# Kernel tuning notes

Measured on AMD Instinct MI355X. Metric: run time of the kernel, lower is better.

Reference implementation:

```python
import jax, jax.numpy as jnp
import numpy as np

# Image grid matching params nImgX/nImgY; nImgZ == nDctY (slice-wise 2D parallel-beam BP)
NIMG_X = 512
NIMG_Y = 512


def _backproject(proj):
    """Pixel-driven 2D parallel-beam backprojection applied per slice.

    proj: (nView, Z, nDct) sinogram (views over [0, pi), unit detector/pixel spacing,
    detector and image both centered). Returns vol: (Z, NIMG_Y, NIMG_X),
    scaled by pi/nView (the weighting the original module applies, cf. its backward).
    """
    nView, Z, nDct = proj.shape
    thetas = jnp.arange(nView, dtype=jnp.float32) * (np.pi / nView)
    xs = jnp.arange(NIMG_X, dtype=jnp.float32) - (NIMG_X - 1) / 2.0
    ys = jnp.arange(NIMG_Y, dtype=jnp.float32) - (NIMG_Y - 1) / 2.0
    ctr = (nDct - 1) / 2.0

    def step(vol, inp):
        p, c, s = inp                      # p: (Z, nDct)
        t = xs[None, :] * c + ys[:, None] * s + ctr   # (Y, X) detector coordinate
        i0 = jnp.floor(t).astype(jnp.int32)
        w = t - i0.astype(jnp.float32)
        v0 = (i0 >= 0) & (i0 < nDct)
        v1 = ((i0 + 1) >= 0) & ((i0 + 1) < nDct)
        i0c = jnp.clip(i0, 0, nDct - 1)
        i1c = jnp.clip(i0 + 1, 0, nDct - 1)
        g0 = p[:, i0c]                      # (Z, Y, X) gather
        g1 = p[:, i1c]
        contrib = g0 * jnp.where(v0, 1.0 - w, 0.0)[None] + g1 * jnp.where(v1, w, 0.0)[None]
        return vol + contrib, None

    vol0 = jnp.zeros((Z, NIMG_Y, NIMG_X), dtype=proj.dtype)
    vol, _ = jax.lax.scan(step, vol0, (proj, jnp.cos(thetas), jnp.sin(thetas)))
    return vol * jnp.float32(np.pi / nView)


def setup_inputs() -> dict:
    key = jax.random.key(0)
    # sinogram: (nDctY=32 slices, 1, nView=720, nDctX=1024)
    x = jax.random.normal(key, (32, 1, 720, 1024), dtype=jnp.float32)
    return {"x": x}


def reference(x):
    # original: squeeze -> (Z, nView, nDct) -> transpose(1,0,2) -> (nView, Z, nDct)
    proj = jnp.transpose(x[:, 0], (1, 0, 2))
    vol = _backproject(proj)               # (Z, NIMG_Y, NIMG_X)
    return vol[:, None, :, :]              # (nImgZ, 1, nImgY, nImgX)
```

## Files before the change

### kernel.cpp

```cpp
#include <hip/hip_runtime.h>
#include <math.h>

#define NVIEW 720
#define NDCT  1024
#define NZ    32
#define NX    512
#define NY    512

#define NR 24
#define RSTRIDE 20

typedef unsigned int uint;

#if __has_builtin(__builtin_amdgcn_fdot2)
#define USE_FDOT2 1
typedef _Float16 half2v __attribute__((ext_vector_type(2)));
#else
#define USE_FDOT2 0
#endif

__device__ __forceinline__ uint f2bf_rne(float f) {
    uint u = __float_as_uint(f);
    return (u + 0x7fffu + ((u >> 16) & 1u)) >> 16;
}

__device__ __forceinline__ uint pack_word(float a, float b) {
#if USE_FDOT2
    union { _Float16 h[2]; uint u; } r;
    r.h[0] = (_Float16)a;
    r.h[1] = (_Float16)(b - a);
    return r.u;
#else
    uint lo = f2bf_rne(b - a);
    uint u  = (f2bf_rne(a) << 16) | lo;
    uint up = u + 0x10000u, um = u - 0x10000u;
    float e0 = fabsf(__uint_as_float(u)  - a);
    float e1 = fabsf(__uint_as_float(up) - a);
    float e2 = fabsf(__uint_as_float(um) - a);
    if (e1 < e0) { u = up; e0 = e1; }
    if (e2 < e0) { u = um; }
    return u;
#endif
}

__global__ __launch_bounds__(64) void pack_kernel(const float* __restrict__ x,
                                                  uint* __restrict__ packed) {
    __shared__ uint tr[64 * 33];
    const int l  = threadIdx.x;
    const int v  = blockIdx.x;
    const int ib = blockIdx.y * 64;
    const bool last = (ib + 64 >= NDCT);
    const float* rowbase = x + (size_t)v * NDCT + ib;

    float pre = 0.0f;
    if (l < NZ && !last) pre = rowbase[(size_t)l * (NVIEW * NDCT) + 64];

    for (int z = 0; z < NZ; ++z) {
        const float* r = rowbase + (size_t)z * (NVIEW * NDCT);
        float a   = r[l];
        float a64 = __shfl(pre, z);
        float b   = __shfl(a, l + 1);
        if (l == 63) b = a64;
        tr[l * 33 + z] = pack_word(a, b);
    }
    __syncthreads();

    uint* obase = packed + ((size_t)v * NDCT + ib) * 32;
    #pragma unroll
    for (int it = 0; it < 8; ++it) {
        int c  = it * 64 + l;
        int il = c >> 3;
        int zc = (c & 7) * 4;
        uint4 w4;
        w4.x = tr[il * 33 + zc + 0];
        w4.y = tr[il * 33 + zc + 1];
        w4.z = tr[il * 33 + zc + 2];
        w4.w = tr[il * 33 + zc + 3];
        *(uint4*)(obase + (size_t)c * 4) = w4;
    }
}

#if USE_FDOT2
#define SAMP(A, zz, uu, WP, WF) do { \
    union { uint q; half2v h; } _c; _c.q = (uu); \
    A[zz] = __builtin_amdgcn_fdot2(_c.h, (WP), A[zz], false); \
} while (0)
#else
#define SAMP(A, zz, uu, WP, WF) do { \
    A[zz] += __uint_as_float(uu); \
    A[zz]  = fmaf((WF), __uint_as_float((uu) << 16), A[zz]); \
} while (0)
#endif

#define SAMPLE16(A, WP, WF) do { \
    SAMP(A, 0, q0.x, WP, WF); SAMP(A, 1, q0.y, WP, WF); \
    SAMP(A, 2, q0.z, WP, WF); SAMP(A, 3, q0.w, WP, WF); \
    SAMP(A, 4, q1.x, WP, WF); SAMP(A, 5, q1.y, WP, WF); \
    SAMP(A, 6, q1.z, WP, WF); SAMP(A, 7, q1.w, WP, WF); \
    SAMP(A, 8, q2.x, WP, WF); SAMP(A, 9, q2.y, WP, WF); \
    SAMP(A,10, q2.z, WP, WF); SAMP(A,11, q2.w, WP, WF); \
    SAMP(A,12, q3.x, WP, WF); SAMP(A,13, q3.y, WP, WF); \
    SAMP(A,14, q3.z, WP, WF); SAMP(A,15, q3.w, WP, WF); \
} while (0)

__global__ __launch_bounds__(128, 4) void bp_lds(const uint* __restrict__ packed,
                                                 float* __restrict__ out) {
    __shared__ float4 tab[NVIEW];
    __shared__ __align__(16) uint stage[2][NR * RSTRIDE];

    const int tid = threadIdx.y * 8 + threadIdx.x;
    const int g   = blockIdx.z;
    const float xf0 = (float)(int)(blockIdx.x * 16) - 255.5f;
    const float yf0 = (float)(int)(blockIdx.y * 16) - 255.5f;

    for (int v = tid; v < NVIEW; v += 128) {
        float th = (float)v * (float)(M_PI / NVIEW);
        float s, c;
        sincosf(th, &s, &c);
        float b0 = fmaf(yf0, s, 511.5f);
        float b1 = fmaf(yf0 + 15.0f, s, 511.5f);
        float t00 = fmaf(xf0, c, b0);
        float t10 = fmaf(xf0 + 15.0f, c, b0);
        float t01 = fmaf(xf0, c, b1);
        float t11 = fmaf(xf0 + 15.0f, c, b1);
        int imin = (int)fminf(fminf(t00, t10), fminf(t01, t11));
        tab[v] = make_float4(c, s, 511.5f - (float)imin, __int_as_float(imin));
    }
    __syncthreads();

    const int x0 = blockIdx.x * 16 + threadIdx.x * 2;
    const int y  = blockIdx.y * 16 + threadIdx.y;
    const float xf = (float)x0 - 255.5f;
    const float yf = (float)y  - 255.5f;

    float acc0[16], acc1[16];
    #pragma unroll
    for (int z = 0; z < 16; ++z) { acc0[z] = 0.0f; acc1[z] = 0.0f; }

    const int  wv   = tid >> 6;
    const int  ln   = tid & 63;
    const bool sact = (ln < 48);
    const int  slot = wv * 48 + ln;
    const int  sr   = slot >> 2;
    const int  sch  = slot & 3;
    const size_t sg_off = ((size_t)sr << 5) + (g << 4) + (sch << 2);
    const int  swr  = sr * RSTRIDE + (sch << 2);

    float4 t4 = tab[0];
    uint4 st;
    if (sact) {
        st = *(const uint4*)(packed + ((size_t)__float_as_int(t4.w) << 5) + sg_off);
        *(uint4*)&stage[0][swr] = st;
    }
    __syncthreads();

    #pragma unroll 2
    for (int v = 0; v < NVIEW; ++v) {
        float4 t4n = t4;
        if (v + 1 < NVIEW) t4n = tab[v + 1];
        if (sact && v + 1 < NVIEW) {
            st = *(const uint4*)(packed + ((size_t)(v + 1) << 15)
                                 + ((size_t)__float_as_int(t4n.w) << 5) + sg_off);
        }

        const float c = t4.x;
        float t0 = fmaf(xf, c, fmaf(yf, t4.y, t4.z));
        float t1 = t0 + c;
        int   i0 = (int)t0;
        int   i1 = (int)t1;
        float w0 = t0 - (float)i0;
        float w1 = t1 - (float)i1;

#if USE_FDOT2
        half2v wp0; wp0[0] = (_Float16)1.0f; wp0[1] = (_Float16)w0;
        half2v wp1; wp1[0] = (_Float16)1.0f; wp1[1] = (_Float16)w1;
#else
        const int wp0 = 0, wp1 = 0;
#endif

        const uint* sp = stage[v & 1] + i0 * RSTRIDE;
        uint4 q0 = *(const uint4*)(sp);
        uint4 q1 = *(const uint4*)(sp + 4);
        uint4 q2 = *(const uint4*)(sp + 8);
        uint4 q3 = *(const uint4*)(sp + 12);

        SAMPLE16(acc0, wp0, w0);

        if (i1 != i0) {
            const uint* sp1 = stage[v & 1] + i1 * RSTRIDE;
            q0 = *(const uint4*)(sp1);
            q1 = *(const uint4*)(sp1 + 4);
            q2 = *(const uint4*)(sp1 + 8);
            q3 = *(const uint4*)(sp1 + 12);
        }

        SAMPLE16(acc1, wp1, w1);

        if (sact && v + 1 < NVIEW) *(uint4*)&stage[(v + 1) & 1][swr] = st;
        __syncthreads();
        t4 = t4n;
    }

    const float scale = 0.0043633231299858236f;
    #pragma unroll
    for (int lz = 0; lz < 16; ++lz) {
        float2 o = make_float2(acc0[lz] * scale, acc1[lz] * scale);
        *(float2*)(out + (((size_t)(g * 16 + lz)) * NY + y) * NX + x0) = o;
    }
}

__global__ __launch_bounds__(256) void bp_direct(const float* __restrict__ xin,
                                                 float* __restrict__ out) {
    __shared__ float2 cs[NVIEW];
    int lt = threadIdx.y * 64 + threadIdx.x;
    for (int v = lt; v < NVIEW; v += 256) {
        float th = (float)v * (float)(M_PI / NVIEW);
        float s, c;
        sincosf(th, &s, &c);
        cs[v] = make_float2(c, s);
    }
    __syncthreads();

    int x = blockIdx.x * 64 + threadIdx.x;
    int y = blockIdx.y * 4 + threadIdx.y;
    float xf = (float)x - 255.5f;
    float yf = (float)y - 255.5f;

    float acc[NZ];
    #pragma unroll
    for (int z = 0; z < NZ; ++z) acc[z] = 0.0f;

    for (int v = 0; v < NVIEW; ++v) {
        float2 a = cs[v];
        float t  = fmaf(xf, a.x, fmaf(yf, a.y, 511.5f));
        int   i0 = (int)t;
        float w  = t - (float)i0;
        const float* p = xin + (size_t)v * NDCT + i0;
        #pragma unroll
        for (int z = 0; z < NZ; ++z) {
            float g0 = p[(size_t)z * NVIEW * NDCT];
            float g1 = p[(size_t)z * NVIEW * NDCT + 1];
            acc[z] += fmaf(w, g1 - g0, g0);
        }
    }

    const float scale = 0.0043633231299858236f;
    #pragma unroll
    for (int z = 0; z < NZ; ++z) {
        out[((size_t)z * NY + y) * NX + x] = acc[z] * scale;
    }
}

extern "C" void kernel_launch(void* const* d_in, const int* in_sizes, int n_in,
                              void* d_out, int out_size, void* d_ws, size_t ws_size,
                              hipStream_t stream) {
    const float* x = (const float*)d_in[0];
    float* out = (float*)d_out;

    const size_t packed_bytes = (size_t)NVIEW * NDCT * NZ * sizeof(uint);

    if (ws_size >= packed_bytes) {
        uint* packed = (uint*)d_ws;
        pack_kernel<<<dim3(NVIEW, NDCT / 64), 64, 0, stream>>>(x, packed);
        bp_lds<<<dim3(NX / 16, NY / 16, 2), dim3(8, 16), 0, stream>>>(packed, out);
    } else {
        bp_direct<<<dim3(NX / 64, NY / 4), dim3(64, 4), 0, stream>>>(x, out);
    }
}
```

Before: 629.4 us.

## Prefetch next view's second-tap samples from global into registers

Computes the next view's detector indices and weights one iteration ahead. When a pixel's second tap falls in a different detector row, the 64 bytes for that row are loaded straight from the packed global buffer into registers instead of being read from the LDS stage. A select then replaces the conditional second LDS read. This aims to overlap index math and load latency with the accumulation loop. The cost is 16 or more extra VGPRs under a 4-wave occupancy bound, plus extra divergent global loads on many iterations.

```diff
diff --git a/kernel.cpp b/kernel.cpp
--- a/kernel.cpp
+++ b/kernel.cpp
@@ -150,7 +150,35 @@
     uint4 st;
     if (sact) {
         st = *(const uint4*)(packed + ((size_t)__float_as_int(t4.w) << 5) + sg_off);
-        *(uint4*)&stage[0][swr] = st;
+    }
+
+    int   i0c, i1c, spoffc;
+    float w0c, w1c;
+#if USE_FDOT2
+    half2v wp0c, wp1c;
+#endif
+    uint4 p0 = {0,0,0,0}, p1 = {0,0,0,0}, p2 = {0,0,0,0}, p3 = {0,0,0,0};
+
+    {
+        const float c = t4.x;
+        float t0 = fmaf(xf, c, fmaf(yf, t4.y, t4.z));
+        float t1 = t0 + c;
+        i0c = (int)t0; i1c = (int)t1;
+        w0c = t0 - (float)i0c; w1c = t1 - (float)i1c;
+#if USE_FDOT2
+        wp0c[0] = (_Float16)1.0f; wp0c[1] = (_Float16)w0c;
+        wp1c[0] = (_Float16)1.0f; wp1c[1] = (_Float16)w1c;
+#endif
+        spoffc = i0c * RSTRIDE;
+        if (i1c != i0c) {
+            const uint* pp = packed + ((size_t)(__float_as_int(t4.w) + i1c) << 5)
+                                    + ((size_t)g << 4);
+            p0 = *(const uint4*)(pp);
+            p1 = *(const uint4*)(pp + 4);
+            p2 = *(const uint4*)(pp + 8);
+            p3 = *(const uint4*)(pp + 12);
+        }
+        if (sact) *(uint4*)&stage[0][swr] = st;
     }
     __syncthreads();
 
@@ -163,38 +191,54 @@
                                  + ((size_t)__float_as_int(t4n.w) << 5) + sg_off);
         }
 
-        const float c = t4.x;
-        float t0 = fmaf(xf, c, fmaf(yf, t4.y, t4.z));
-        float t1 = t0 + c;
-        int   i0 = (int)t0;
-        int   i1 = (int)t1;
-        float w0 = t0 - (float)i0;
-        float w1 = t1 - (float)i1;
-
-#if USE_FDOT2
-        half2v wp0; wp0[0] = (_Float16)1.0f; wp0[1] = (_Float16)w0;
-        half2v wp1; wp1[0] = (_Float16)1.0f; wp1[1] = (_Float16)w1;
-#else
-        const int wp0 = 0, wp1 = 0;
-#endif
-
-        const uint* sp = stage[v & 1] + i0 * RSTRIDE;
+        const uint* sp = stage[v & 1] + spoffc;
         uint4 q0 = *(const uint4*)(sp);
         uint4 q1 = *(const uint4*)(sp + 4);
         uint4 q2 = *(const uint4*)(sp + 8);
         uint4 q3 = *(const uint4*)(sp + 12);
 
-        SAMPLE16(acc0, wp0, w0);
-
-        if (i1 != i0) {
-            const uint* sp1 = stage[v & 1] + i1 * RSTRIDE;
-            q0 = *(const uint4*)(sp1);
-            q1 = *(const uint4*)(sp1 + 4);
-            q2 = *(const uint4*)(sp1 + 8);
-            q3 = *(const uint4*)(sp1 + 12);
-        }
-
-        SAMPLE16(acc1, wp1, w1);
+        SAMPLE16(acc0, wp0c, w0c);
+
+        {
+            const bool m = (i1c != i0c);
+            q0.x = m ? p0.x : q0.x; q0.y = m ? p0.y : q0.y;
+            q0.z = m ? p0.z : q0.z; q0.w = m ? p0.w : q0.w;
+            q1.x = m ? p1.x : q1.x; q1.y = m ? p1.y : q1.y;
+            q1.z = m ? p1.z : q1.z; q1.w = m ? p1.w : q1.w;
+            q2.x = m ? p2.x : q2.x; q2.y = m ? p2.y : q2.y;
+            q2.z = m ? p2.z : q2.z; q2.w = m ? p2.w : q2.w;
+            q3.x = m ? p3.x : q3.x; q3.y = m ? p3.y : q3.y;
+            q3.z = m ? p3.z : q3.z; q3.w = m ? p3.w : q3.w;
+        }
+
+        SAMPLE16(acc1, wp1c, w1c);
+
+        if (v + 1 < NVIEW) {
+            const float cn = t4n.x;
+            float t0n = fmaf(xf, cn, fmaf(yf, t4n.y, t4n.z));
+            float t1n = t0n + cn;
+            int i0n = (int)t0n, i1n = (int)t1n;
+            float w0n = t0n - (float)i0n, w1n = t1n - (float)i1n;
+#if USE_FDOT2
+            half2v wp0n, wp1n;
+            wp0n[0] = (_Float16)1.0f; wp0n[1] = (_Float16)w0n;
+            wp1n[0] = (_Float16)1.0f; wp1n[1] = (_Float16)w1n;
+#endif
+            if (i1n != i0n) {
+                const uint* pp = packed + ((size_t)(v + 1) << 15)
+                                 + ((size_t)(__float_as_int(t4n.w) + i1n) << 5)
+                                 + ((size_t)g << 4);
+                p0 = *(const uint4*)(pp);
+                p1 = *(const uint4*)(pp + 4);
+                p2 = *(const uint4*)(pp + 8);
+                p3 = *(const uint4*)(pp + 12);
+            }
+            i0c = i0n; i1c = i1n; w0c = w0n; w1c = w1n;
+#if USE_FDOT2
+            wp0c = wp0n; wp1c = wp1n;
+#endif
+            spoffc = i0n * RSTRIDE;
+        }
 
         if (sact && v + 1 < NVIEW) *(uint4*)&stage[(v + 1) & 1][swr] = st;
         __syncthreads();
```

After: 1.807 ms. 187% more time.

## Compute 2x2 pixel quads per thread in single-wave blocks without barriers

Applied to the files above, without the earlier changes.

Replaces the 128-thread backprojection kernel with a single-wavefront kernel where each thread accumulates a 2x2 pixel quad, visiting the quad's detector bins in an order chosen by view angle so LDS row gathers are reused when bins coincide. Because the block is one wavefront, the per-view __syncthreads barriers are dropped and staging is split across all 64 lanes. This aims to cut LDS read traffic per sample and barrier stalls. In exchange it uses more accumulator registers, which lowers occupancy, and it relies on in-wave LDS ordering instead of explicit synchronization.

```diff
diff --git a/kernel.cpp b/kernel.cpp
--- a/kernel.cpp
+++ b/kernel.cpp
@@ -103,17 +103,25 @@
     SAMP(A,14, q3.z, WP, WF); SAMP(A,15, q3.w, WP, WF); \
 } while (0)
 
-__global__ __launch_bounds__(128, 4) void bp_lds(const uint* __restrict__ packed,
+#define GATHER(SB, IR) do { \
+    const uint* _sp = (SB) + (IR) * RSTRIDE; \
+    q0 = *(const uint4*)(_sp); \
+    q1 = *(const uint4*)(_sp + 4); \
+    q2 = *(const uint4*)(_sp + 8); \
+    q3 = *(const uint4*)(_sp + 12); \
+} while (0)
+
+__global__ __launch_bounds__(64, 2) void bp_quad(const uint* __restrict__ packed,
                                                  float* __restrict__ out) {
     __shared__ float4 tab[NVIEW];
     __shared__ __align__(16) uint stage[2][NR * RSTRIDE];
 
-    const int tid = threadIdx.y * 8 + threadIdx.x;
+    const int tid = threadIdx.x;
     const int g   = blockIdx.z;
     const float xf0 = (float)(int)(blockIdx.x * 16) - 255.5f;
     const float yf0 = (float)(int)(blockIdx.y * 16) - 255.5f;
 
-    for (int v = tid; v < NVIEW; v += 128) {
+    for (int v = tid; v < NVIEW; v += 64) {
         float th = (float)v * (float)(M_PI / NVIEW);
         float s, c;
         sincosf(th, &s, &c);
@@ -126,86 +134,100 @@
         int imin = (int)fminf(fminf(t00, t10), fminf(t01, t11));
         tab[v] = make_float4(c, s, 511.5f - (float)imin, __int_as_float(imin));
     }
-    __syncthreads();
-
-    const int x0 = blockIdx.x * 16 + threadIdx.x * 2;
-    const int y  = blockIdx.y * 16 + threadIdx.y;
-    const float xf = (float)x0 - 255.5f;
-    const float yf = (float)y  - 255.5f;
-
-    float acc0[16], acc1[16];
-    #pragma unroll
-    for (int z = 0; z < 16; ++z) { acc0[z] = 0.0f; acc1[z] = 0.0f; }
-
-    const int  wv   = tid >> 6;
-    const int  ln   = tid & 63;
-    const bool sact = (ln < 48);
-    const int  slot = wv * 48 + ln;
-    const int  sr   = slot >> 2;
-    const int  sch  = slot & 3;
-    const size_t sg_off = ((size_t)sr << 5) + (g << 4) + (sch << 2);
-    const int  swr  = sr * RSTRIDE + (sch << 2);
+
+    const int qx = tid & 7, qy = tid >> 3;
+    const int xo = blockIdx.x * 16 + qx * 2;
+    const int yo = blockIdx.y * 16 + qy * 2;
+    const float xf = (float)xo - 255.5f;
+    const float yf = (float)yo - 255.5f;
+
+    float a00[16], a10[16], a01[16], a11[16];
+    #pragma unroll
+    for (int z = 0; z < 16; ++z) { a00[z] = 0.0f; a10[z] = 0.0f; a01[z] = 0.0f; a11[z] = 0.0f; }
+
+    const int  sr0  = tid >> 2, sch0 = tid & 3;
+    const size_t sg0 = ((size_t)sr0 << 5) + (g << 4) + (sch0 << 2);
+    const int  ld0  = sr0 * RSTRIDE + (sch0 << 2);
+    const size_t sg1 = sg0 + ((size_t)16 << 5);
+    const int  ld1  = ld0 + 16 * RSTRIDE;
+    const bool s2   = (tid < 32);
 
     float4 t4 = tab[0];
-    uint4 st;
-    if (sact) {
-        st = *(const uint4*)(packed + ((size_t)__float_as_int(t4.w) << 5) + sg_off);
-        *(uint4*)&stage[0][swr] = st;
-    }
-    __syncthreads();
+    {
+        const uint* vb = packed + ((size_t)__float_as_int(t4.w) << 5);
+        uint4 st0 = *(const uint4*)(vb + sg0);
+        uint4 st1;
+        if (s2) st1 = *(const uint4*)(vb + sg1);
+        *(uint4*)&stage[0][ld0] = st0;
+        if (s2) *(uint4*)&stage[0][ld1] = st1;
+    }
 
     #pragma unroll 2
     for (int v = 0; v < NVIEW; ++v) {
         float4 t4n = t4;
         if (v + 1 < NVIEW) t4n = tab[v + 1];
-        if (sact && v + 1 < NVIEW) {
-            st = *(const uint4*)(packed + ((size_t)(v + 1) << 15)
-                                 + ((size_t)__float_as_int(t4n.w) << 5) + sg_off);
-        }
-
-        const float c = t4.x;
-        float t0 = fmaf(xf, c, fmaf(yf, t4.y, t4.z));
-        float t1 = t0 + c;
-        int   i0 = (int)t0;
-        int   i1 = (int)t1;
-        float w0 = t0 - (float)i0;
-        float w1 = t1 - (float)i1;
+        uint4 st0, st1;
+        if (v + 1 < NVIEW) {
+            const uint* vb = packed + ((size_t)(v + 1) << 15)
+                           + ((size_t)__float_as_int(t4n.w) << 5);
+            st0 = *(const uint4*)(vb + sg0);
+            if (s2) st1 = *(const uint4*)(vb + sg1);
+        }
+
+        const float c = t4.x, s = t4.y;
+        float t00 = fmaf(xf, c, fmaf(yf, s, t4.z));
+        float t10 = t00 + c;
+        float t01 = t00 + s;
+        float t11 = t10 + s;
+        int   i00 = (int)t00, i10 = (int)t10, i01 = (int)t01, i11 = (int)t11;
+        float w00 = t00 - (float)i00, w10 = t10 - (float)i10;
+        float w01 = t01 - (float)i01, w11 = t11 - (float)i11;
 
 #if USE_FDOT2
-        half2v wp0; wp0[0] = (_Float16)1.0f; wp0[1] = (_Float16)w0;
-        half2v wp1; wp1[0] = (_Float16)1.0f; wp1[1] = (_Float16)w1;
-#else
-        const int wp0 = 0, wp1 = 0;
-#endif
-
-        const uint* sp = stage[v & 1] + i0 * RSTRIDE;
-        uint4 q0 = *(const uint4*)(sp);
-        uint4 q1 = *(const uint4*)(sp + 4);
-        uint4 q2 = *(const uint4*)(sp + 8);
-        uint4 q3 = *(const uint4*)(sp + 12);
-
-        SAMPLE16(acc0, wp0, w0);
-
-        if (i1 != i0) {
-            const uint* sp1 = stage[v & 1] + i1 * RSTRIDE;
-            q0 = *(const uint4*)(sp1);
-            q1 = *(const uint4*)(sp1 + 4);
-            q2 = *(const uint4*)(sp1 + 8);
-            q3 = *(const uint4*)(sp1 + 12);
-        }
-
-        SAMPLE16(acc1, wp1, w1);
-
-        if (sact && v + 1 < NVIEW) *(uint4*)&stage[(v + 1) & 1][swr] = st;
-        __syncthreads();
+        half2v wp00, wp10, wp01, wp11;
+        wp00[0] = (_Float16)1.0f; wp00[1] = (_Float16)w00;
+        wp10[0] = (_Float16)1.0f; wp10[1] = (_Float16)w10;
+        wp01[0] = (_Float16)1.0f; wp01[1] = (_Float16)w01;
+        wp11[0] = (_Float16)1.0f; wp11[1] = (_Float16)w11;
+#else
+        const int wp00 = 0, wp10 = 0, wp01 = 0, wp11 = 0;
+#endif
+
+        const uint* sb = stage[v & 1];
+        uint4 q0, q1, q2, q3;
+        int ir = i00;
+        GATHER(sb, ir);
+        SAMPLE16(a00, wp00, w00);
+        if (fabsf(c) <= fabsf(s)) {
+            if (i10 != ir) { ir = i10; GATHER(sb, ir); }
+            SAMPLE16(a10, wp10, w10);
+            if (i11 != ir) { ir = i11; GATHER(sb, ir); }
+            SAMPLE16(a11, wp11, w11);
+            if (i01 != ir) { ir = i01; GATHER(sb, ir); }
+            SAMPLE16(a01, wp01, w01);
+        } else {
+            if (i01 != ir) { ir = i01; GATHER(sb, ir); }
+            SAMPLE16(a01, wp01, w01);
+            if (i11 != ir) { ir = i11; GATHER(sb, ir); }
+            SAMPLE16(a11, wp11, w11);
+            if (i10 != ir) { ir = i10; GATHER(sb, ir); }
+            SAMPLE16(a10, wp10, w10);
+        }
+
+        if (v + 1 < NVIEW) {
+            uint* pb = &stage[(v + 1) & 1][0];
+            *(uint4*)(pb + ld0) = st0;
+            if (s2) *(uint4*)(pb + ld1) = st1;
+        }
         t4 = t4n;
     }
 
     const float scale = 0.0043633231299858236f;
     #pragma unroll
     for (int lz = 0; lz < 16; ++lz) {
-        float2 o = make_float2(acc0[lz] * scale, acc1[lz] * scale);
-        *(float2*)(out + (((size_t)(g * 16 + lz)) * NY + y) * NX + x0) = o;
+        size_t base = (((size_t)(g * 16 + lz)) * NY + yo) * NX + xo;
+        *(float2*)(out + base)      = make_float2(a00[lz] * scale, a10[lz] * scale);
+        *(float2*)(out + base + NX) = make_float2(a01[lz] * scale, a11[lz] * scale);
     }
 }
 
@@ -262,7 +284,7 @@
     if (ws_size >= packed_bytes) {
         uint* packed = (uint*)d_ws;
         pack_kernel<<<dim3(NVIEW, NDCT / 64), 64, 0, stream>>>(x, packed);
-        bp_lds<<<dim3(NX / 16, NY / 16, 2), dim3(8, 16), 0, stream>>>(packed, out);
+        bp_quad<<<dim3(NX / 16, NY / 16, 2), dim3(64), 0, stream>>>(packed, out);
     } else {
         bp_direct<<<dim3(NX / 64, NY / 4), dim3(64, 4), 0, stream>>>(x, out);
     }
```

Measured after the change: 761.9 us. 1.21x slower.

## Pack two z-slices per fp16x2 word and interpolate with v_fma_mix

Applied to the files above, without the earlier changes.

The packed sinogram changes from one word per (detector, z) holding value and delta to one fp16x2 word holding two z-slices. This halves the workspace size, the global staging traffic and the LDS footprint. The inner loop loads adjacent detector rows and uses inline-asm v_fma_mix_f32 with weights (1-w, w) to do the lerp, reusing the shared row between the two pixels depending on the sign of cos. This doubles the mix-FMA instructions per sample compared with fdot2. It also stores raw fp16 values instead of a delta, which can change precision.

```diff
diff --git a/kernel.cpp b/kernel.cpp
--- a/kernel.cpp
+++ b/kernel.cpp
@@ -7,106 +7,75 @@
 #define NX    512
 #define NY    512
 
-#define NR 24
-#define RSTRIDE 20
+#define NR  24
+#define RS16 12
 
 typedef unsigned int uint;
 
-#if __has_builtin(__builtin_amdgcn_fdot2)
-#define USE_FDOT2 1
-typedef _Float16 half2v __attribute__((ext_vector_type(2)));
-#else
-#define USE_FDOT2 0
-#endif
-
-__device__ __forceinline__ uint f2bf_rne(float f) {
-    uint u = __float_as_uint(f);
-    return (u + 0x7fffu + ((u >> 16) & 1u)) >> 16;
-}
-
-__device__ __forceinline__ uint pack_word(float a, float b) {
-#if USE_FDOT2
+#define MIXLO(ACC, U, WF) \
+    asm("v_fma_mix_f32 %0, %1, %2, %0 op_sel:[0,0,0] op_sel_hi:[1,0,0]" \
+        : "+v"(ACC) : "v"(U), "v"(WF))
+#define MIXHI(ACC, U, WF) \
+    asm("v_fma_mix_f32 %0, %1, %2, %0 op_sel:[1,0,0] op_sel_hi:[1,0,0]" \
+        : "+v"(ACC) : "v"(U), "v"(WF))
+
+#define MIXPAIR(A0, A1, UA, UB, VV, WW) do { \
+    MIXLO(A0, UA, VV); MIXLO(A0, UB, WW); \
+    MIXHI(A1, UA, VV); MIXHI(A1, UB, WW); \
+} while (0)
+
+#define PXSAMPLE(ACC, RA0, RA1, RB0, RB1, VV, WW) do { \
+    MIXPAIR(ACC[ 0], ACC[ 1], RA0.x, RB0.x, VV, WW); \
+    MIXPAIR(ACC[ 2], ACC[ 3], RA0.y, RB0.y, VV, WW); \
+    MIXPAIR(ACC[ 4], ACC[ 5], RA0.z, RB0.z, VV, WW); \
+    MIXPAIR(ACC[ 6], ACC[ 7], RA0.w, RB0.w, VV, WW); \
+    MIXPAIR(ACC[ 8], ACC[ 9], RA1.x, RB1.x, VV, WW); \
+    MIXPAIR(ACC[10], ACC[11], RA1.y, RB1.y, VV, WW); \
+    MIXPAIR(ACC[12], ACC[13], RA1.z, RB1.z, VV, WW); \
+    MIXPAIR(ACC[14], ACC[15], RA1.w, RB1.w, VV, WW); \
+} while (0)
+
+__device__ __forceinline__ uint packh2(float a, float b) {
     union { _Float16 h[2]; uint u; } r;
     r.h[0] = (_Float16)a;
-    r.h[1] = (_Float16)(b - a);
+    r.h[1] = (_Float16)b;
     return r.u;
-#else
-    uint lo = f2bf_rne(b - a);
-    uint u  = (f2bf_rne(a) << 16) | lo;
-    uint up = u + 0x10000u, um = u - 0x10000u;
-    float e0 = fabsf(__uint_as_float(u)  - a);
-    float e1 = fabsf(__uint_as_float(up) - a);
-    float e2 = fabsf(__uint_as_float(um) - a);
-    if (e1 < e0) { u = up; e0 = e1; }
-    if (e2 < e0) { u = um; }
-    return u;
-#endif
-}
-
-__global__ __launch_bounds__(64) void pack_kernel(const float* __restrict__ x,
-                                                  uint* __restrict__ packed) {
-    __shared__ uint tr[64 * 33];
+}
+
+__global__ __launch_bounds__(64) void pack16_kernel(const float* __restrict__ x,
+                                                    uint* __restrict__ packed) {
+    __shared__ uint tr[64 * 17];
     const int l  = threadIdx.x;
     const int v  = blockIdx.x;
     const int ib = blockIdx.y * 64;
-    const bool last = (ib + 64 >= NDCT);
     const float* rowbase = x + (size_t)v * NDCT + ib;
 
-    float pre = 0.0f;
-    if (l < NZ && !last) pre = rowbase[(size_t)l * (NVIEW * NDCT) + 64];
-
-    for (int z = 0; z < NZ; ++z) {
-        const float* r = rowbase + (size_t)z * (NVIEW * NDCT);
-        float a   = r[l];
-        float a64 = __shfl(pre, z);
-        float b   = __shfl(a, l + 1);
-        if (l == 63) b = a64;
-        tr[l * 33 + z] = pack_word(a, b);
-    }
-    __syncthreads();
-
-    uint* obase = packed + ((size_t)v * NDCT + ib) * 32;
-    #pragma unroll
-    for (int it = 0; it < 8; ++it) {
+    for (int zp = 0; zp < 16; ++zp) {
+        float a0 = rowbase[(size_t)(2 * zp)     * (NVIEW * NDCT) + l];
+        float a1 = rowbase[(size_t)(2 * zp + 1) * (NVIEW * NDCT) + l];
+        tr[l * 17 + zp] = packh2(a0, a1);
+    }
+    __syncthreads();
+
+    uint* obase = packed + ((size_t)v * NDCT + ib) * 16;
+    #pragma unroll
+    for (int it = 0; it < 4; ++it) {
         int c  = it * 64 + l;
-        int il = c >> 3;
-        int zc = (c & 7) * 4;
+        int il = c >> 2;
+        int zp = (c & 3) * 4;
         uint4 w4;
-        w4.x = tr[il * 33 + zc + 0];
-        w4.y = tr[il * 33 + zc + 1];
-        w4.z = tr[il * 33 + zc + 2];
-        w4.w = tr[il * 33 + zc + 3];
+        w4.x = tr[il * 17 + zp + 0];
+        w4.y = tr[il * 17 + zp + 1];
+        w4.z = tr[il * 17 + zp + 2];
+        w4.w = tr[il * 17 + zp + 3];
         *(uint4*)(obase + (size_t)c * 4) = w4;
     }
 }
 
-#if USE_FDOT2
-#define SAMP(A, zz, uu, WP, WF) do { \
-    union { uint q; half2v h; } _c; _c.q = (uu); \
-    A[zz] = __builtin_amdgcn_fdot2(_c.h, (WP), A[zz], false); \
-} while (0)
-#else
-#define SAMP(A, zz, uu, WP, WF) do { \
-    A[zz] += __uint_as_float(uu); \
-    A[zz]  = fmaf((WF), __uint_as_float((uu) << 16), A[zz]); \
-} while (0)
-#endif
-
-#define SAMPLE16(A, WP, WF) do { \
-    SAMP(A, 0, q0.x, WP, WF); SAMP(A, 1, q0.y, WP, WF); \
-    SAMP(A, 2, q0.z, WP, WF); SAMP(A, 3, q0.w, WP, WF); \
-    SAMP(A, 4, q1.x, WP, WF); SAMP(A, 5, q1.y, WP, WF); \
-    SAMP(A, 6, q1.z, WP, WF); SAMP(A, 7, q1.w, WP, WF); \
-    SAMP(A, 8, q2.x, WP, WF); SAMP(A, 9, q2.y, WP, WF); \
-    SAMP(A,10, q2.z, WP, WF); SAMP(A,11, q2.w, WP, WF); \
-    SAMP(A,12, q3.x, WP, WF); SAMP(A,13, q3.y, WP, WF); \
-    SAMP(A,14, q3.z, WP, WF); SAMP(A,15, q3.w, WP, WF); \
-} while (0)
-
-__global__ __launch_bounds__(128, 4) void bp_lds(const uint* __restrict__ packed,
-                                                 float* __restrict__ out) {
+__global__ __launch_bounds__(128, 4) void bp_lds16(const uint* __restrict__ packed,
+                                                   float* __restrict__ out) {
     __shared__ float4 tab[NVIEW];
-    __shared__ __align__(16) uint stage[2][NR * RSTRIDE];
+    __shared__ __align__(16) uint stage[2][NR * RS16];
 
     const int tid = threadIdx.y * 8 + threadIdx.x;
     const int g   = blockIdx.z;
@@ -139,17 +108,17 @@
 
     const int  wv   = tid >> 6;
     const int  ln   = tid & 63;
-    const bool sact = (ln < 48);
-    const int  slot = wv * 48 + ln;
-    const int  sr   = slot >> 2;
-    const int  sch  = slot & 3;
-    const size_t sg_off = ((size_t)sr << 5) + (g << 4) + (sch << 2);
-    const int  swr  = sr * RSTRIDE + (sch << 2);
+    const bool sact = (ln < 24);
+    const int  slot = wv * 24 + ln;
+    const int  sr   = slot >> 1;
+    const int  sch  = slot & 1;
+    const size_t sg_off = ((size_t)sr << 4) + (g << 3) + (sch << 2);
+    const int  swr  = sr * RS16 + (sch << 2);
 
     float4 t4 = tab[0];
     uint4 st;
     if (sact) {
-        st = *(const uint4*)(packed + ((size_t)__float_as_int(t4.w) << 5) + sg_off);
+        st = *(const uint4*)(packed + ((size_t)__float_as_int(t4.w) << 4) + sg_off);
         *(uint4*)&stage[0][swr] = st;
     }
     __syncthreads();
@@ -159,42 +128,45 @@
         float4 t4n = t4;
         if (v + 1 < NVIEW) t4n = tab[v + 1];
         if (sact && v + 1 < NVIEW) {
-            st = *(const uint4*)(packed + ((size_t)(v + 1) << 15)
-                                 + ((size_t)__float_as_int(t4n.w) << 5) + sg_off);
+            st = *(const uint4*)(packed + ((size_t)(v + 1) << 14)
+                                 + ((size_t)__float_as_int(t4n.w) << 4) + sg_off);
         }
 
-        const float c = t4.x;
-        float t0 = fmaf(xf, c, fmaf(yf, t4.y, t4.z));
+        const float c = t4.x, s = t4.y;
+        float t0 = fmaf(xf, c, fmaf(yf, s, t4.z));
         float t1 = t0 + c;
         int   i0 = (int)t0;
         int   i1 = (int)t1;
         float w0 = t0 - (float)i0;
         float w1 = t1 - (float)i1;
-
-#if USE_FDOT2
-        half2v wp0; wp0[0] = (_Float16)1.0f; wp0[1] = (_Float16)w0;
-        half2v wp1; wp1[0] = (_Float16)1.0f; wp1[1] = (_Float16)w1;
-#else
-        const int wp0 = 0, wp1 = 0;
-#endif
-
-        const uint* sp = stage[v & 1] + i0 * RSTRIDE;
-        uint4 q0 = *(const uint4*)(sp);
-        uint4 q1 = *(const uint4*)(sp + 4);
-        uint4 q2 = *(const uint4*)(sp + 8);
-        uint4 q3 = *(const uint4*)(sp + 12);
-
-        SAMPLE16(acc0, wp0, w0);
-
-        if (i1 != i0) {
-            const uint* sp1 = stage[v & 1] + i1 * RSTRIDE;
-            q0 = *(const uint4*)(sp1);
-            q1 = *(const uint4*)(sp1 + 4);
-            q2 = *(const uint4*)(sp1 + 8);
-            q3 = *(const uint4*)(sp1 + 12);
+        float v0 = 1.0f - w0;
+        float v1 = 1.0f - w1;
+
+        const uint* sp = stage[v & 1] + i0 * RS16;
+        uint4 ra0 = *(const uint4*)(sp);
+        uint4 ra1 = *(const uint4*)(sp + 4);
+        uint4 rb0 = *(const uint4*)(sp + RS16);
+        uint4 rb1 = *(const uint4*)(sp + RS16 + 4);
+
+        PXSAMPLE(acc0, ra0, ra1, rb0, rb1, v0, w0);
+
+        if (c >= 0.0f) {
+            if (i1 != i0) {
+                ra0 = rb0; ra1 = rb1;
+                const uint* s2 = stage[v & 1] + (i1 + 1) * RS16;
+                rb0 = *(const uint4*)(s2);
+                rb1 = *(const uint4*)(s2 + 4);
+            }
+        } else {
+            if (i1 != i0) {
+                rb0 = ra0; rb1 = ra1;
+                const uint* s2 = stage[v & 1] + i1 * RS16;
+                ra0 = *(const uint4*)(s2);
+                ra1 = *(const uint4*)(s2 + 4);
+            }
         }
 
-        SAMPLE16(acc1, wp1, w1);
+        PXSAMPLE(acc1, ra0, ra1, rb0, rb1, v1, w1);
 
         if (sact && v + 1 < NVIEW) *(uint4*)&stage[(v + 1) & 1][swr] = st;
         __syncthreads();
@@ -257,12 +229,12 @@
     const float* x = (const float*)d_in[0];
     float* out = (float*)d_out;
 
-    const size_t packed_bytes = (size_t)NVIEW * NDCT * NZ * sizeof(uint);
+    const size_t packed_bytes = (size_t)NVIEW * NDCT * 16 * sizeof(uint);
 
     if (ws_size >= packed_bytes) {
         uint* packed = (uint*)d_ws;
-        pack_kernel<<<dim3(NVIEW, NDCT / 64), 64, 0, stream>>>(x, packed);
-        bp_lds<<<dim3(NX / 16, NY / 16, 2), dim3(8, 16), 0, stream>>>(packed, out);
+        pack16_kernel<<<dim3(NVIEW, NDCT / 64), 64, 0, stream>>>(x, packed);
+        bp_lds16<<<dim3(NX / 16, NY / 16, 2), dim3(8, 16), 0, stream>>>(packed, out);
     } else {
         bp_direct<<<dim3(NX / 64, NY / 4), dim3(64, 4), 0, stream>>>(x, out);
     }
```

Result: slower. 876.4 us (+39.3%).
